# Optimization experiments

Hardware: AMD Instinct MI355X
Metric: run time of the kernel (lower is better)

Reference implementation:

```python
import jax, jax.numpy as jnp
import numpy as np

DIM = 1024
HEADS = 16
HEAD_DIM = DIM // HEADS


def apply_rope(x):
    # x: (B, S, H, D)
    B, S, H, D = x.shape
    half = D // 2
    freqs = 1.0 / (10000.0 ** (jnp.arange(half, dtype=jnp.float32) / half))
    pos = jnp.arange(S, dtype=jnp.float32)
    angles = pos[:, None] * freqs[None, :]          # (S, half)
    sin = jnp.sin(angles)[None, :, None, :]
    cos = jnp.cos(angles)[None, :, None, :]
    x1, x2 = x[..., :half], x[..., half:]
    return jnp.concatenate([x1 * cos - x2 * sin, x1 * sin + x2 * cos], axis=-1)


def setup_inputs() -> dict:
    key = jax.random.key(0)
    ks = jax.random.split(key, 5)
    x = jax.random.normal(ks[0], (2, 2048, DIM), dtype=jnp.float32)
    s = 1.0 / np.sqrt(DIM)
    qkv_w = jax.random.uniform(ks[1], (3 * DIM, DIM), minval=-s, maxval=s, dtype=jnp.float32)
    qkv_b = jax.random.uniform(ks[2], (3 * DIM,), minval=-s, maxval=s, dtype=jnp.float32)
    proj_w = jax.random.uniform(ks[3], (DIM, DIM), minval=-s, maxval=s, dtype=jnp.float32)
    proj_b = jax.random.uniform(ks[4], (DIM,), minval=-s, maxval=s, dtype=jnp.float32)
    return {"x": x, "qkv_w": qkv_w, "qkv_b": qkv_b, "proj_w": proj_w, "proj_b": proj_b}


def reference(x, qkv_w, qkv_b, proj_w, proj_b):
    B, S, D = x.shape
    qkv = x @ qkv_w.T + qkv_b                       # (B, S, 3D)
    q, k, v = jnp.split(qkv, 3, axis=-1)
    q = q.reshape(B, S, HEADS, HEAD_DIM)
    k = k.reshape(B, S, HEADS, HEAD_DIM)
    v = v.reshape(B, S, HEADS, HEAD_DIM)
    q = apply_rope(q)
    k = apply_rope(k)
    scale = 1.0 / np.sqrt(HEAD_DIM)
    attn = jnp.einsum('bqhd,bkhd->bhqk', q, k) * scale
    mask = jnp.triu(jnp.ones((S, S), dtype=bool), k=1)
    attn = jnp.where(mask[None, None], -1e9, attn)
    attn = jax.nn.softmax(attn, axis=-1)
    out = jnp.einsum('bhqk,bkhd->bqhd', attn, v).reshape(B, S, D)
    return out @ proj_w.T + proj_b
```

## Files before the change

kernel.cpp:

```cpp
#include <hip/hip_runtime.h>
#include <hip/hip_bf16.h>
#include <stdint.h>

typedef unsigned short u16;
typedef __attribute__((ext_vector_type(8))) short bf16x8;
typedef __attribute__((ext_vector_type(4))) float f32x4;
typedef __attribute__((ext_vector_type(16))) float f32x16;

typedef __attribute__((address_space(1))) const void gas_t;
typedef __attribute__((address_space(3))) void las_t;

#define DEV __device__ __forceinline__

DEV float bf2f(u16 v){ union{uint32_t u; float f;} x; x.u = ((uint32_t)v)<<16; return x.f; }
DEV u16 f2bf(float f){ union{float f; uint32_t u;} x; x.f=f; uint32_t r = x.u + 0x7fff + ((x.u>>16)&1u); return (u16)(r>>16); }

DEV uint32_t pk2(float a, float b){
  return (uint32_t)f2bf(a) | ((uint32_t)f2bf(b)<<16);
}

DEV uint32_t cvtpk(float a, float b){
  uint32_t r;
  asm("v_cvt_pk_bf16_f32 %0, %1, %2" : "=v"(r) : "v"(a), "v"(b));
  return r;
}

DEV void xswap(uint32_t a, uint32_t b, int hi, uint32_t& ra, uint32_t& rb){
#if __has_builtin(__builtin_amdgcn_permlane32_swap)
  auto r = __builtin_amdgcn_permlane32_swap((int)a, (int)b, false, false);
  ra = (uint32_t)r[0]; rb = (uint32_t)r[1];
#else
  uint32_t sa = (uint32_t)__shfl_xor((int)a, 32);
  uint32_t sb = (uint32_t)__shfl_xor((int)b, 32);
  ra = hi ? sb : a;
  rb = hi ? b  : sa;
#endif
}

DEV void gload_lds16(const u16* g, u16* l){
  __builtin_amdgcn_global_load_lds((gas_t*)g, (las_t*)l, 16, 0, 0);
}

__global__ void cvt_f32_bf16(const float* __restrict__ src, u16* __restrict__ dst, int n4){
  int i = blockIdx.x*blockDim.x + threadIdx.x;
  if(i < n4){
    float4 v = ((const float4*)src)[i];
    ushort4 o; o.x=f2bf(v.x); o.y=f2bf(v.y); o.z=f2bf(v.z); o.w=f2bf(v.w);
    ((ushort4*)dst)[i] = o;
  }
}

template<int OUT_F32>
__global__ __launch_bounds__(256,2)
void gemm_bt(const u16* __restrict__ A, const u16* __restrict__ Bw,
             const float* __restrict__ bias, void* __restrict__ Cp, int N)
{
  constexpr int BK = 32, KSTEPS = 1024/BK;
  __shared__ __align__(16) u16 As[128][BK];
  __shared__ __align__(16) u16 Bs[128][BK];
  const int tid = threadIdx.x, w = tid>>6, l = tid&63;
  const int a = l&15, g = l>>4;
  const int m0 = blockIdx.y*128, n0 = blockIdx.x*128;
  const int wr = w>>1, wc = w&1;
  f32x4 zero = {0.f,0.f,0.f,0.f};
  f32x4 acc[4][4];
  #pragma unroll
  for(int m=0;m<4;m++) for(int n=0;n<4;n++) acc[m][n]=zero;

  const int srow = l>>2, scol = (l&3)*8;
  const u16* Ag = A  + (size_t)(m0 + w*32 + srow)*1024 + scol;
  const u16* Bg = Bw + (size_t)(n0 + w*32 + srow)*1024 + scol;

  for(int kt=0; kt<KSTEPS; ++kt){
    if(kt) __syncthreads();
    gload_lds16(Ag + kt*BK,           &As[w*32   ][0]);
    gload_lds16(Ag + kt*BK + 16*1024, &As[w*32+16][0]);
    gload_lds16(Bg + kt*BK,           &Bs[w*32   ][0]);
    gload_lds16(Bg + kt*BK + 16*1024, &Bs[w*32+16][0]);
    __syncthreads();
    bf16x8 af[4], bf[4];
    #pragma unroll
    for(int m=0;m<4;m++) af[m] = *(const bf16x8*)&As[wr*64 + m*16 + a][g*8];
    #pragma unroll
    for(int n=0;n<4;n++) bf[n] = *(const bf16x8*)&Bs[wc*64 + n*16 + a][g*8];
    #pragma unroll
    for(int m=0;m<4;m++)
      #pragma unroll
      for(int n=0;n<4;n++)
        acc[m][n] = __builtin_amdgcn_mfma_f32_16x16x32_bf16(af[m], bf[n], acc[m][n], 0,0,0);
  }
  #pragma unroll
  for(int n=0;n<4;n++){
    int col = n0 + wc*64 + n*16 + a;
    float bv = bias[col];
    #pragma unroll
    for(int m=0;m<4;m++){
      int row = m0 + wr*64 + m*16 + g*4;
      #pragma unroll
      for(int r=0;r<4;r++){
        float v = acc[m][n][r] + bv;
        if(OUT_F32) ((float*)Cp)[(size_t)(row+r)*N + col] = v;
        else        ((u16*)Cp)[(size_t)(row+r)*N + col] = f2bf(v);
      }
    }
  }
}

__global__ void rope_relayout(const u16* __restrict__ qkv, u16* __restrict__ q_r,
                              u16* __restrict__ k_r)
{
  int t = blockIdx.x*256 + threadIdx.x;
  int gI = t&3, h=(t>>2)&15, row=t>>6;
  int s = row & 2047, b = row >> 11;
  int d0 = gI*8;
  const float QSC = 0.18033688011112042f;
  const u16* base = qkv + (size_t)row*3072 + h*64 + d0;
  union U { uint4 v; u16 e[8]; };
  U q1,q2,k1,k2, oq1,oq2,ok1,ok2;
  q1.v = *(const uint4*)(base);
  q2.v = *(const uint4*)(base+32);
  k1.v = *(const uint4*)(base+1024);
  k2.v = *(const uint4*)(base+1024+32);
  #pragma unroll
  for(int j=0;j<8;j++){
    float d = (float)(d0+j);
    float fr = __expf(-0.28782313662425574f * d);
    float ang = (float)s * fr;
    float sn, cs; sincosf(ang, &sn, &cs);
    float snq = sn*QSC, csq = cs*QSC;
    float x1 = bf2f(q1.e[j]), x2 = bf2f(q2.e[j]);
    oq1.e[j] = f2bf(x1*csq - x2*snq); oq2.e[j] = f2bf(x1*snq + x2*csq);
    x1 = bf2f(k1.e[j]); x2 = bf2f(k2.e[j]);
    ok1.e[j] = f2bf(x1*cs - x2*sn); ok2.e[j] = f2bf(x1*sn + x2*cs);
  }
  size_t o = ((size_t)(b*16+h)*2048 + s)*64 + d0;
  *(uint4*)(q_r+o) = oq1.v; *(uint4*)(q_r+o+32) = oq2.v;
  *(uint4*)(k_r+o) = ok1.v; *(uint4*)(k_r+o+32) = ok2.v;
}

__global__ __launch_bounds__(256,2)
void v_transpose(const u16* __restrict__ qkv, u16* __restrict__ vt)
{
  __shared__ uint32_t L[64*65];
  const int tid = threadIdx.x;
  const int bh = blockIdx.x & 31;
  const int stile = blockIdx.x >> 5;
  const int b = bh >> 4, h = bh & 15;
  const int s0 = stile*128;
  const int cg = tid & 7, sr = tid >> 3;
  const u16* src = qkv + (size_t)(b*2048 + s0)*3072 + 2048 + h*64 + cg*8;
  #pragma unroll
  for(int p=0;p<2;p++){
    int srow = p*64 + sr*2;
    union{uint4 v; u16 e[8];} v0, v1;
    v0.v = *(const uint4*)(src + (size_t)srow*3072);
    v1.v = *(const uint4*)(src + (size_t)(srow+1)*3072);
    #pragma unroll
    for(int jj=0;jj<8;jj++)
      L[(cg*8+jj)*65 + p*32 + sr] = (uint32_t)v0.e[jj] | ((uint32_t)v1.e[jj]<<16);
  }
  __syncthreads();
  const int w = tid>>6, ln = tid&63;
  u16* dst = vt + (size_t)bh*64*2048 + s0;
  #pragma unroll
  for(int dd=0;dd<16;dd++){
    int d = w*16 + dd;
    *(uint32_t*)(dst + (size_t)d*2048 + ln*2) = L[d*65 + ln];
  }
}

__global__ __launch_bounds__(256,4)
void attn_fwd8(const u16* __restrict__ Q, const u16* __restrict__ K,
               const u16* __restrict__ VT, u16* __restrict__ O)
{
  __shared__ __align__(16) u16 Ks[2][64][64];
  __shared__ __align__(16) u16 Vs[2][64][64];
  const int tid = threadIdx.x, w = tid>>6, ln = tid&63;
  const int lo = ln&31, hi = ln>>5;
  const int wq = w>>1, wk = w&1;
  const int b0 = blockIdx.x;
  const int bh = b0 & 31;
  const int j64 = 31 - (b0 >> 5);
  const int q0 = j64*64 + wq*32;
  const int nt = j64 + 1;

  const u16* Qb = Q  + ((size_t)bh*2048 + q0)*64;
  const u16* Kb = K  + (size_t)bh*2048*64;
  const u16* Vt = VT + (size_t)bh*64*2048;

  bf16x8 qf[4];
  #pragma unroll
  for(int s=0;s<4;s++) qf[s] = *(const bf16x8*)(Qb + lo*64 + s*16 + hi*8);

  const int rsub = ln>>3;
  const int coloff = ((ln&7) ^ rsub) * 8;
  const int wrow = (w&1)*32;
  const size_t rstride = (w<2) ? 64 : 2048;
  const u16* src0 = (w<2) ? (Kb + (size_t)(wrow+rsub)*64 + coloff)
                          : (Vt + (size_t)(wrow+rsub)*2048 + coloff);
  u16* ldsw = (w<2) ? (&Ks[0][0][0] + wrow*64) : (&Vs[0][0][0] + wrow*64);

  f32x16 oacc0, oacc1, z16;
  #pragma unroll
  for(int r=0;r<16;r++){ oacc0[r]=0.f; oacc1[r]=0.f; z16[r]=0.f; }
  float l_loc = 0.f;
  const int swz = (lo&7)<<4;

  #pragma unroll
  for(int g=0;g<4;g++) gload_lds16(src0 + (size_t)g*8*rstride, ldsw + g*512);
  __syncthreads();

  int buf = 0;
  for(int t=0; t<nt; ++t){
    if(t+1 < nt){
      const size_t koff = (w<2) ? (size_t)(t+1)*64*64 : (size_t)(t+1)*64;
      u16* dst = ldsw + (buf^1)*4096;
      #pragma unroll
      for(int g=0;g<4;g++) gload_lds16(src0 + koff + (size_t)g*8*rstride, dst + g*512);
    }

    const int kv32 = t*64 + wk*32;
    if(kv32 <= q0 + 31){
      const u16* KsB = &Ks[buf][0][0];
      const u16* VsB = &Vs[buf][0][0];
      bf16x8 kf[4], vf[4];
      #pragma unroll
      for(int s=0;s<4;s++)
        kf[s] = *(const bf16x8*)(KsB + (wk*32+lo)*64 + (((s*32 + hi*16) ^ swz)>>1));
      #pragma unroll
      for(int dt=0;dt<2;dt++)
        #pragma unroll
        for(int s2=0;s2<2;s2++)
          vf[dt*2+s2] = *(const bf16x8*)(VsB + (dt*32+lo)*64 + (((wk*64 + s2*32 + hi*16) ^ swz)>>1));

      f32x16 st = __builtin_amdgcn_mfma_f32_32x32x16_bf16(kf[0], qf[0], z16, 0,0,0);
      #pragma unroll
      for(int s=1;s<4;s++)
        st = __builtin_amdgcn_mfma_f32_32x32x16_bf16(kf[s], qf[s], st, 0,0,0);

      float p[16];
      #pragma unroll
      for(int r=0;r<16;r++) p[r] = exp2f(st[r]);
      if(kv32 == q0){
        #pragma unroll
        for(int r=0;r<16;r++){
          const int kvg = (r&3) + 8*(r>>2) + 4*hi;
          p[r] = (kvg <= lo) ? p[r] : 0.f;
        }
      }

      float sm[8];
      #pragma unroll
      for(int i=0;i<8;i++) sm[i] = p[i] + p[i+8];
      #pragma unroll
      for(int s=4;s>=1;s>>=1)
        #pragma unroll
        for(int i=0;i<s;i++) sm[i] += sm[i+s];
      l_loc += sm[0];

      uint32_t pk[8];
      #pragma unroll
      for(int i=0;i<8;i++) pk[i] = cvtpk(p[2*i], p[2*i+1]);

      union PF { bf16x8 v; uint32_t u[4]; } pf0, pf1;
      xswap(pk[0], pk[2], hi, pf0.u[0], pf0.u[2]);
      xswap(pk[1], pk[3], hi, pf0.u[1], pf0.u[3]);
      xswap(pk[4], pk[6], hi, pf1.u[0], pf1.u[2]);
      xswap(pk[5], pk[7], hi, pf1.u[1], pf1.u[3]);

      oacc0 = __builtin_amdgcn_mfma_f32_32x32x16_bf16(vf[0], pf0.v, oacc0, 0,0,0);
      oacc0 = __builtin_amdgcn_mfma_f32_32x32x16_bf16(vf[1], pf1.v, oacc0, 0,0,0);
      oacc1 = __builtin_amdgcn_mfma_f32_32x32x16_bf16(vf[2], pf0.v, oacc1, 0,0,0);
      oacc1 = __builtin_amdgcn_mfma_f32_32x32x16_bf16(vf[3], pf1.v, oacc1, 0,0,0);
    }
    __syncthreads();
    buf ^= 1;
  }

  float l_run = l_loc + __shfl_xor(l_loc, 32);

  float* LoC = (float*)&Ks[0][0][0];
  float* LlC = (float*)&Vs[0][0][0];
  if(wk == 1){
    #pragma unroll
    for(int r=0;r<16;r++){
      const int d = 4*hi + (r&3) + 8*(r>>2);
      LoC[(wq*64 + d   )*32 + lo] = oacc0[r];
      LoC[(wq*64 + d+32)*32 + lo] = oacc1[r];
    }
    if(hi==0) LlC[wq*32 + lo] = l_run;
  }
  __syncthreads();
  if(wk == 0){
    l_run += LlC[wq*32 + lo];
    #pragma unroll
    for(int r=0;r<16;r++){
      const int d = 4*hi + (r&3) + 8*(r>>2);
      oacc0[r] += LoC[(wq*64 + d   )*32 + lo];
      oacc1[r] += LoC[(wq*64 + d+32)*32 + lo];
    }
    const float invl = 1.f / l_run;
    const int row_g = (bh>>4)*2048 + q0 + lo;
    u16* Ob = O + (size_t)row_g*1024 + (bh&15)*64;
    #pragma unroll
    for(int g2=0; g2<4; g2++){
      uint2 pr;
      pr.x = pk2(oacc0[4*g2+0]*invl, oacc0[4*g2+1]*invl);
      pr.y = pk2(oacc0[4*g2+2]*invl, oacc0[4*g2+3]*invl);
      *(uint2*)(Ob + 8*g2 + 4*hi) = pr;
    }
    #pragma unroll
    for(int g2=0; g2<4; g2++){
      uint2 pr;
      pr.x = pk2(oacc1[4*g2+0]*invl, oacc1[4*g2+1]*invl);
      pr.y = pk2(oacc1[4*g2+2]*invl, oacc1[4*g2+3]*invl);
      *(uint2*)(Ob + 32 + 8*g2 + 4*hi) = pr;
    }
  }
}

extern "C" void kernel_launch(void* const* d_in, const int* in_sizes, int n_in,
                              void* d_out, int out_size, void* d_ws, size_t ws_size,
                              hipStream_t stream)
{
  const float* x      = (const float*)d_in[0];
  const float* qkv_w  = (const float*)d_in[1];
  const float* qkv_b  = (const float*)d_in[2];
  const float* proj_w = (const float*)d_in[3];
  const float* proj_b = (const float*)d_in[4];
  float* out = (float*)d_out;
  char* ws = (char*)d_ws;

  u16* xb    = (u16*)(ws);
  u16* wqkv  = (u16*)(ws + 8388608);
  u16* wproj = (u16*)(ws + 8388608 + 6291456);
  u16* qkvr  = (u16*)(ws + 16777216);
  u16* q_r   = (u16*)(ws + 41943040);
  u16* k_r   = q_r + 4194304;
  u16* vt    = k_r + 4194304;
  u16* o_b   = xb;

  cvt_f32_bf16<<<4096,256,0,stream>>>(x, xb, 1048576);
  cvt_f32_bf16<<<3072,256,0,stream>>>(qkv_w, wqkv, 786432);
  cvt_f32_bf16<<<1024,256,0,stream>>>(proj_w, wproj, 262144);

  dim3 gA(24,32);
  gemm_bt<0><<<gA,256,0,stream>>>(xb, wqkv, qkv_b, qkvr, 3072);

  rope_relayout<<<1024,256,0,stream>>>(qkvr, q_r, k_r);
  v_transpose<<<512,256,0,stream>>>(qkvr, vt);

  attn_fwd8<<<1024,256,0,stream>>>(q_r, k_r, vt, o_b);

  dim3 gC(8,32);
  gemm_bt<1><<<gC,256,0,stream>>>(o_b, wproj, proj_b, out, 1024);
}
```

Measured before the change: 121.7 us.

## Triple-buffer GEMM LDS tiles with async prefetch two k-steps ahead

Rewrites the bf16 GEMM main loop to use three LDS buffers, issuing global-to-LDS loads two k-steps ahead and waiting with vmcnt counters instead of syncing twice per step. The aim is to overlap global memory latency with MFMA work and drop one barrier per iteration. It triples LDS use per block and raises the launch-bounds occupancy hint to 3 blocks, which may constrain registers.

```diff
diff --git a/kernel.cpp b/kernel.cpp
--- a/kernel.cpp
+++ b/kernel.cpp
@@ -51,13 +51,13 @@
 }
 
 template<int OUT_F32>
-__global__ __launch_bounds__(256,2)
+__global__ __launch_bounds__(256,3)
 void gemm_bt(const u16* __restrict__ A, const u16* __restrict__ Bw,
              const float* __restrict__ bias, void* __restrict__ Cp, int N)
 {
   constexpr int BK = 32, KSTEPS = 1024/BK;
-  __shared__ __align__(16) u16 As[128][BK];
-  __shared__ __align__(16) u16 Bs[128][BK];
+  __shared__ __align__(16) u16 As[3][128][BK];
+  __shared__ __align__(16) u16 Bs[3][128][BK];
   const int tid = threadIdx.x, w = tid>>6, l = tid&63;
   const int a = l&15, g = l>>4;
   const int m0 = blockIdx.y*128, n0 = blockIdx.x*128;
@@ -71,24 +71,45 @@
   const u16* Ag = A  + (size_t)(m0 + w*32 + srow)*1024 + scol;
   const u16* Bg = Bw + (size_t)(n0 + w*32 + srow)*1024 + scol;
 
+#define STAGE(KIDX, BUF) {                                        \
+    u16* ab = &As[BUF][w*32][0];                                  \
+    u16* bb = &Bs[BUF][w*32][0];                                  \
+    gload_lds16(Ag + (KIDX)*BK,           ab);                    \
+    gload_lds16(Ag + (KIDX)*BK + 16*1024, ab + 16*BK);            \
+    gload_lds16(Bg + (KIDX)*BK,           bb);                    \
+    gload_lds16(Bg + (KIDX)*BK + 16*1024, bb + 16*BK);            \
+  }
+
+  STAGE(0, 0);
+  STAGE(1, 1);
+
+  int bc = 0, bn = 2;
   for(int kt=0; kt<KSTEPS; ++kt){
-    if(kt) __syncthreads();
-    gload_lds16(Ag + kt*BK,           &As[w*32   ][0]);
-    gload_lds16(Ag + kt*BK + 16*1024, &As[w*32+16][0]);
-    gload_lds16(Bg + kt*BK,           &Bs[w*32   ][0]);
-    gload_lds16(Bg + kt*BK + 16*1024, &Bs[w*32+16][0]);
-    __syncthreads();
+    if(kt+1 < KSTEPS) asm volatile("s_waitcnt vmcnt(4)" ::: "memory");
+    else              asm volatile("s_waitcnt vmcnt(0)" ::: "memory");
+    __builtin_amdgcn_s_barrier();
+    __builtin_amdgcn_sched_barrier(0);
+
+    if(kt+2 < KSTEPS) STAGE(kt+2, bn);
+
+    const u16* AsB = &As[bc][0][0];
+    const u16* BsB = &Bs[bc][0][0];
     bf16x8 af[4], bf[4];
     #pragma unroll
-    for(int m=0;m<4;m++) af[m] = *(const bf16x8*)&As[wr*64 + m*16 + a][g*8];
-    #pragma unroll
-    for(int n=0;n<4;n++) bf[n] = *(const bf16x8*)&Bs[wc*64 + n*16 + a][g*8];
+    for(int m=0;m<4;m++) af[m] = *(const bf16x8*)(AsB + (wr*64 + m*16 + a)*BK + g*8);
+    #pragma unroll
+    for(int n=0;n<4;n++) bf[n] = *(const bf16x8*)(BsB + (wc*64 + n*16 + a)*BK + g*8);
     #pragma unroll
     for(int m=0;m<4;m++)
       #pragma unroll
       for(int n=0;n<4;n++)
         acc[m][n] = __builtin_amdgcn_mfma_f32_16x16x32_bf16(af[m], bf[n], acc[m][n], 0,0,0);
-  }
+
+    bc = (bc==2) ? 0 : bc+1;
+    bn = (bn==2) ? 0 : bn+1;
+  }
+#undef STAGE
+
   #pragma unroll
   for(int n=0;n<4;n++){
     int col = n0 + wc*64 + n*16 + a;
```

New measurement: 120.7 us. No clear change (-0.8%).
